# Kernel optimization log

Measured on AMD Instinct MI355X. Metric: run time of the kernel, lower is better.

Reference implementation:

```python
import jax, jax.numpy as jnp
import numpy as np

NPOS_MAX = 64
SCALE = 0.125  # head_dim ** -0.5


def setup_inputs() -> dict:
    key = jax.random.key(0)
    kq, kk, kv, kp, kw = jax.random.split(key, 5)
    B, S, D = 32, 1024, 64
    return {
        "q": jax.random.normal(kq, (B, S, D), dtype=jnp.float32),
        "k": jax.random.normal(kk, (B, S, D), dtype=jnp.float32),
        "v": jax.random.normal(kv, (B, S, D), dtype=jnp.float32),
        "pos_emb": jax.random.normal(kp, (1, D, NPOS_MAX), dtype=jnp.float32) * 0.02,
        "w_k": jax.random.normal(kw, (1, D, D), dtype=jnp.float32) * 0.02,
        "is_cope_k": 1,
    }


def reference(q, k, v, pos_emb, w_k, is_cope_k):
    # mode == 0: plain scaled QK^T
    attn_logits = jnp.einsum("bqd,bkd->bqk", q * SCALE, k)  # [B,S,S]
    gates = jax.nn.sigmoid(attn_logits)
    # reverse cumulative sum along the key axis (flip-cumsum-flip)
    pos = jnp.cumsum(gates[..., ::-1], axis=-1)[..., ::-1]
    pos = jnp.minimum(pos, NPOS_MAX - 1)
    pos_ceil = jnp.ceil(pos).astype(jnp.int32)
    pos_floor = jnp.floor(pos).astype(jnp.int32)
    base = q if is_cope_k else k
    logits_int = jnp.einsum("bsd,odn->bsn", base, pos_emb)  # [B,S,npos]
    logits_ceil = jnp.take_along_axis(logits_int, pos_ceil, axis=-1)
    logits_floor = jnp.take_along_axis(logits_int, pos_floor, axis=-1)
    w = pos - pos_floor.astype(pos.dtype)
    return logits_ceil * w + logits_floor * (1.0 - w)
```

## Files before the change

kernel.cpp:

```cpp
#include <hip/hip_runtime.h>

#define SLEN 1024
#define DDIM 64
#define NPOS 64
#define QROWS 16
#define QCOLS 256
#define COPE_SCALE 0.125f
#define GSTR 260
#define TSTR 66

typedef __bf16 bf16x8 __attribute__((ext_vector_type(8)));
typedef float f32x4 __attribute__((ext_vector_type(4)));

__device__ __forceinline__ unsigned short f2bf_hi(float x) {
    unsigned u = __builtin_bit_cast(unsigned, x);
    unsigned r = u + 0x7FFFu + ((u >> 16) & 1u);
    return (unsigned short)(r >> 16);
}
__device__ __forceinline__ float bf2f(unsigned short h) {
    unsigned u = ((unsigned)h) << 16;
    return __builtin_bit_cast(float, u);
}
struct U8 { ushort4 a, b; };
__device__ __forceinline__ bf16x8 pack8(const unsigned short* s) {
    U8 u = {{s[0], s[1], s[2], s[3]}, {s[4], s[5], s[6], s[7]}};
    return __builtin_bit_cast(bf16x8, u);
}

__global__ __launch_bounds__(256) void prep_kernel(
    const float* __restrict__ k,
    unsigned short* __restrict__ khi,
    unsigned short* __restrict__ klo,
    int n4)
{
    int i = blockIdx.x * 256 + threadIdx.x;
    if (i >= n4) return;
    float4 v = ((const float4*)k)[i];
    ushort4 h, l;
    h.x = f2bf_hi(v.x); l.x = f2bf_hi(v.x - bf2f(h.x));
    h.y = f2bf_hi(v.y); l.y = f2bf_hi(v.y - bf2f(h.y));
    h.z = f2bf_hi(v.z); l.z = f2bf_hi(v.z - bf2f(h.z));
    h.w = f2bf_hi(v.w); l.w = f2bf_hi(v.w - bf2f(h.w));
    ((ushort4*)khi)[i] = h;
    ((ushort4*)klo)[i] = l;
}

__global__ __launch_bounds__(256, 6) void cope_mfma_kernel(
    const float* __restrict__ q,
    const float* __restrict__ k,
    const float* __restrict__ pos_emb,
    const int*   __restrict__ is_cope_k,
    const unsigned short* __restrict__ khi,
    const unsigned short* __restrict__ klo,
    float*       __restrict__ out)
{
    __shared__ __align__(16) float G[QROWS * GSTR];
    __shared__ __align__(16) float tableL[QROWS * TSTR];
    __shared__ float Racc[QROWS];

    const int t = threadIdx.x;
    const int wave = t >> 6;
    const int lane = t & 63;
    const int quad = lane >> 4;
    const int nloc = lane & 15;
    const int blk = blockIdx.x;
    const int batch = blk >> 6;
    const int qbase = (blk & 63) * QROWS;

    if (t < QROWS) Racc[t] = 0.f;

    bf16x8 a_hi[2], a_lo[2];
    {
        const float* qrow = q + (size_t)(batch * SLEN + qbase + nloc) * DDIM + quad * 8;
        #pragma unroll
        for (int ks = 0; ks < 2; ++ks) {
            float4 v0 = *(const float4*)(qrow + ks * 32);
            float4 v1 = *(const float4*)(qrow + ks * 32 + 4);
            float xs[8] = {v0.x, v0.y, v0.z, v0.w, v1.x, v1.y, v1.z, v1.w};
            unsigned short hb[8], lb[8];
            #pragma unroll
            for (int j = 0; j < 8; ++j) {
                hb[j] = f2bf_hi(xs[j]);
                lb[j] = f2bf_hi(xs[j] - bf2f(hb[j]));
            }
            a_hi[ks] = pack8(hb);
            a_lo[ks] = pack8(lb);
        }
    }

    {
        const int icope = *is_cope_k;
        bf16x8 t_hi[2], t_lo[2];
        if (icope) {
            t_hi[0] = a_hi[0]; t_hi[1] = a_hi[1];
            t_lo[0] = a_lo[0]; t_lo[1] = a_lo[1];
        } else {
            size_t boff = (size_t)(batch * SLEN + qbase + nloc) * DDIM + quad * 8;
            t_hi[0] = __builtin_bit_cast(bf16x8, *(const uint4*)(khi + boff));
            t_hi[1] = __builtin_bit_cast(bf16x8, *(const uint4*)(khi + boff + 32));
            t_lo[0] = __builtin_bit_cast(bf16x8, *(const uint4*)(klo + boff));
            t_lo[1] = __builtin_bit_cast(bf16x8, *(const uint4*)(klo + boff + 32));
        }
        bf16x8 p_hi[2];
        #pragma unroll
        for (int ks = 0; ks < 2; ++ks) {
            unsigned short hb[8];
            #pragma unroll
            for (int j = 0; j < 8; ++j) {
                float pv = pos_emb[(quad * 8 + j + ks * 32) * NPOS + wave * 16 + nloc];
                hb[j] = f2bf_hi(pv);
            }
            p_hi[ks] = pack8(hb);
        }
        f32x4 tacc = {0.f, 0.f, 0.f, 0.f};
        tacc = __builtin_amdgcn_mfma_f32_16x16x32_bf16(t_hi[0], p_hi[0], tacc, 0, 0, 0);
        tacc = __builtin_amdgcn_mfma_f32_16x16x32_bf16(t_lo[0], p_hi[0], tacc, 0, 0, 0);
        tacc = __builtin_amdgcn_mfma_f32_16x16x32_bf16(t_hi[1], p_hi[1], tacc, 0, 0, 0);
        tacc = __builtin_amdgcn_mfma_f32_16x16x32_bf16(t_lo[1], p_hi[1], tacc, 0, 0, 0);
        #pragma unroll
        for (int reg = 0; reg < 4; ++reg)
            tableL[(quad * 4 + reg) * TSTR + wave * 16 + nloc] = tacc[reg];
    }

    int remaining = 0;
    for (int qi = 3; qi >= 0; --qi) {
        #pragma unroll
        for (int i = 0; i < 4; ++i) {
            const int tl = wave * 4 + i;
            size_t boff = (size_t)(batch * SLEN + qi * QCOLS + tl * 16 + nloc) * DDIM + quad * 8;
            uint4 bh0 = *(const uint4*)(khi + boff);
            uint4 bh1 = *(const uint4*)(khi + boff + 32);
            uint4 bl0 = *(const uint4*)(klo + boff);
            uint4 bl1 = *(const uint4*)(klo + boff + 32);
            f32x4 acc = {0.f, 0.f, 0.f, 0.f};
            acc = __builtin_amdgcn_mfma_f32_16x16x32_bf16(a_hi[0], __builtin_bit_cast(bf16x8, bh0), acc, 0, 0, 0);
            acc = __builtin_amdgcn_mfma_f32_16x16x32_bf16(a_lo[0], __builtin_bit_cast(bf16x8, bh0), acc, 0, 0, 0);
            acc = __builtin_amdgcn_mfma_f32_16x16x32_bf16(a_hi[0], __builtin_bit_cast(bf16x8, bl0), acc, 0, 0, 0);
            acc = __builtin_amdgcn_mfma_f32_16x16x32_bf16(a_hi[1], __builtin_bit_cast(bf16x8, bh1), acc, 0, 0, 0);
            acc = __builtin_amdgcn_mfma_f32_16x16x32_bf16(a_lo[1], __builtin_bit_cast(bf16x8, bh1), acc, 0, 0, 0);
            acc = __builtin_amdgcn_mfma_f32_16x16x32_bf16(a_hi[1], __builtin_bit_cast(bf16x8, bl1), acc, 0, 0, 0);
            #pragma unroll
            for (int reg = 0; reg < 4; ++reg) {
                float x = acc[reg] * COPE_SCALE;
                float g = __builtin_amdgcn_rcpf(1.0f + __expf(-x));
                G[(quad * 4 + reg) * GSTR + tl * 16 + nloc] = g;
            }
        }
        __syncthreads();

        #pragma unroll
        for (int rep = 0; rep < 4; ++rep) {
            const int row = wave * 4 + rep;
            const float roff = Racc[row];
            float4 gv = *(const float4*)&G[row * GSTR + lane * 4];
            float ls3 = gv.w;
            float ls2 = gv.z + ls3;
            float ls1 = gv.y + ls2;
            float ls0 = gv.x + ls1;
            const float T = ls0;
            float v = T;
            #pragma unroll
            for (int ofs = 1; ofs < 64; ofs <<= 1) {
                float u = __shfl_down(v, ofs);
                if (lane + ofs < 64) v += u;
            }
            if (lane == 0) Racc[row] = roff + v;
            const float E = (v - T) + roff;

            const float tabv = tableL[row * TSTR + lane];
            float dtabv = __shfl_down(tabv, 1) - tabv;
            if (lane == 63) dtabv = 0.f;
            float ls[4] = {ls0, ls1, ls2, ls3};
            float res[4];
            #pragma unroll
            for (int i = 0; i < 4; ++i) {
                float p = ls[i] + E;
                p = fminf(p, (float)(NPOS - 1));
                float pf = floorf(p);
                int fi = (int)pf;
                float w = p - pf;
                float tf = __shfl(tabv, fi);
                float td = __shfl(dtabv, fi);
                res[i] = tf + w * td;
            }
            float* orow = out + (size_t)(batch * SLEN + qbase + row) * SLEN + qi * QCOLS + lane * 4;
            f32x4 o = {res[0], res[1], res[2], res[3]};
            __builtin_nontemporal_store(o, (f32x4*)orow);
        }
        __syncthreads();

        float mn = Racc[0];
        #pragma unroll
        for (int r = 1; r < QROWS; ++r) mn = fminf(mn, Racc[r]);
        if (mn >= (float)(NPOS - 1)) { remaining = qi; break; }
    }

    if (remaining > 0) {
        const int ncols = remaining * QCOLS;
        #pragma unroll
        for (int rep = 0; rep < 4; ++rep) {
            const int row = wave * 4 + rep;
            const float v63 = tableL[row * TSTR + (NPOS - 1)];
            f32x4 bv = {v63, v63, v63, v63};
            float* orow = out + (size_t)(batch * SLEN + qbase + row) * SLEN;
            for (int c = lane * 4; c < ncols; c += 256)
                __builtin_nontemporal_store(bv, (f32x4*)(orow + c));
        }
    }
}

#define KTILE 128
#define KPAD 68
#define NTILES (SLEN / KTILE)
#define FQROWS 8

__global__ __launch_bounds__(256) void cope_fallback(
    const float* __restrict__ q,
    const float* __restrict__ k,
    const float* __restrict__ pos_emb,
    const int*   __restrict__ is_cope_k,
    float*       __restrict__ out)
{
    __shared__ __align__(16) float smem[KTILE * KPAD];
    __shared__ __align__(16) float qT[DDIM][FQROWS];
    __shared__ __align__(16) float baseT[DDIM][FQROWS];
    __shared__ __align__(16) float tableL2[FQROWS][NPOS];

    const int t = threadIdx.x;
    const int blk = blockIdx.x;
    const int batch = blk / (SLEN / FQROWS);
    const int qbase = (blk % (SLEN / FQROWS)) * FQROWS;
    const float* bsrc = (*is_cope_k) ? q : k;

    for (int i = t; i < FQROWS * DDIM; i += 256) {
        int r = i >> 6, d = i & 63;
        size_t gi = (size_t)(batch * SLEN + qbase + r) * DDIM + d;
        qT[d][r] = q[gi];
        baseT[d][r] = bsrc[gi];
    }
    __syncthreads();
    for (int i = t; i < FQROWS * NPOS; i += 256) {
        int r = i >> 6, n = i & 63;
        float a = 0.f;
        #pragma unroll
        for (int d = 0; d < DDIM; ++d) a += baseT[d][r] * pos_emb[d * NPOS + n];
        tableL2[r][n] = a;
    }
    const int jl = t & 127;
    const int qg = t >> 7;
    float acc[4][NTILES];
    #pragma unroll
    for (int r = 0; r < 4; ++r)
        #pragma unroll
        for (int tl = 0; tl < NTILES; ++tl) acc[r][tl] = 0.f;
    float (*kT)[KPAD] = (float (*)[KPAD])smem;
    const float* kbatch = k + (size_t)batch * SLEN * DDIM;
    #pragma unroll
    for (int tile = 0; tile < NTILES; ++tile) {
        __syncthreads();
        const float4* src = (const float4*)(kbatch + tile * KTILE * DDIM);
        #pragma unroll
        for (int i = 0; i < (KTILE * DDIM / 4) / 256; ++i) {
            int idx = i * 256 + t;
            int row = (idx * 4) >> 6;
            int col = (idx * 4) & 63;
            float4 vv = src[idx];
            *(float4*)&kT[row][col] = vv;
        }
        __syncthreads();
        #pragma unroll
        for (int d = 0; d < DDIM; d += 4) {
            float4 kv = *(const float4*)&kT[jl][d];
            float4 q0 = *(const float4*)&qT[d + 0][qg * 4];
            float4 q1 = *(const float4*)&qT[d + 1][qg * 4];
            float4 q2 = *(const float4*)&qT[d + 2][qg * 4];
            float4 q3 = *(const float4*)&qT[d + 3][qg * 4];
            acc[0][tile] += kv.x * q0.x + kv.y * q1.x + kv.z * q2.x + kv.w * q3.x;
            acc[1][tile] += kv.x * q0.y + kv.y * q1.y + kv.z * q2.y + kv.w * q3.y;
            acc[2][tile] += kv.x * q0.z + kv.y * q1.z + kv.z * q2.z + kv.w * q3.z;
            acc[3][tile] += kv.x * q0.w + kv.y * q1.w + kv.z * q2.w + kv.w * q3.w;
        }
    }
    __syncthreads();
    float (*G2)[SLEN] = (float (*)[SLEN])smem;
    #pragma unroll
    for (int r = 0; r < 4; ++r)
        #pragma unroll
        for (int tl = 0; tl < NTILES; ++tl) {
            float x = acc[r][tl] * COPE_SCALE;
            G2[qg * 4 + r][tl * KTILE + jl] = 1.0f / (1.0f + __expf(-x));
        }
    __syncthreads();
    const int wave = t >> 6;
    const int lane = t & 63;
    #pragma unroll
    for (int rep = 0; rep < 2; ++rep) {
        const int row = wave * 2 + rep;
        float g4[4][4];
        #pragma unroll
        for (int s = 0; s < 4; ++s) {
            float4 v = *(const float4*)&G2[row][s * 256 + lane * 4];
            g4[s][0] = v.x; g4[s][1] = v.y; g4[s][2] = v.z; g4[s][3] = v.w;
        }
        float ls[4][4], T[4];
        #pragma unroll
        for (int s = 0; s < 4; ++s) {
            float a = 0.f;
            #pragma unroll
            for (int i = 3; i >= 0; --i) { a += g4[s][i]; ls[s][i] = a; }
            T[s] = a;
        }
        float E[4], Stot[4];
        #pragma unroll
        for (int s = 0; s < 4; ++s) {
            float v = T[s];
            #pragma unroll
            for (int ofs = 1; ofs < 64; ofs <<= 1) {
                float u = __shfl_down(v, ofs);
                if (lane + ofs < 64) v += u;
            }
            E[s] = v - T[s];
            Stot[s] = __shfl(v, 0);
        }
        float segOff[4];
        segOff[3] = 0.f;
        segOff[2] = Stot[3];
        segOff[1] = Stot[3] + Stot[2];
        segOff[0] = Stot[3] + Stot[2] + Stot[1];
        const float* tab = tableL2[row];
        float* orow = out + (size_t)(batch * SLEN + qbase + row) * SLEN;
        #pragma unroll
        for (int s = 0; s < 4; ++s) {
            float res[4];
            #pragma unroll
            for (int i = 0; i < 4; ++i) {
                float p = ls[s][i] + E[s] + segOff[s];
                p = fminf(p, (float)(NPOS - 1));
                float pf = floorf(p);
                int fi = (int)pf;
                int ci = (int)ceilf(p);
                float w = p - pf;
                res[i] = tab[ci] * w + tab[fi] * (1.0f - w);
            }
            float4 o; o.x = res[0]; o.y = res[1]; o.z = res[2]; o.w = res[3];
            *(float4*)&orow[s * 256 + lane * 4] = o;
        }
    }
}

extern "C" void kernel_launch(void* const* d_in, const int* in_sizes, int n_in,
                              void* d_out, int out_size, void* d_ws, size_t ws_size,
                              hipStream_t stream) {
    const float* q        = (const float*)d_in[0];
    const float* k        = (const float*)d_in[1];
    const float* pos_emb  = (const float*)d_in[3];
    const int*   is_cope_k = (const int*)d_in[5];
    float* out = (float*)d_out;

    const int nk = in_sizes[1];
    const int B = in_sizes[0] / (SLEN * DDIM);
    const size_t ws_need = (size_t)nk * 2 * sizeof(unsigned short);

    if (ws_size >= ws_need) {
        unsigned short* khi = (unsigned short*)d_ws;
        unsigned short* klo = khi + nk;
        int n4 = nk / 4;
        prep_kernel<<<(n4 + 255) / 256, 256, 0, stream>>>(k, khi, klo, n4);
        cope_mfma_kernel<<<B * (SLEN / QROWS), 256, 0, stream>>>(
            q, k, pos_emb, is_cope_k, khi, klo, out);
    } else {
        cope_fallback<<<B * (SLEN / FQROWS), 256, 0, stream>>>(
            q, k, pos_emb, is_cope_k, out);
    }
}
```

Baseline: 173.8 us.

## Prep only last key quarter; split remaining keys to bf16 inline from fp32

The prep kernel now converts only the final 256-key chunk of each batch into hi/lo bf16 arrays instead of all keys. The main kernel splits the other chunks on the fly from fp32 k, and only when the early-exit check has not already fired. When is_cope_k is 0, the table base is also split inline from fp32. This cuts prep work and workspace traffic, since most chunks are usually skipped. The cost is extra VALU conversion work and twice-as-wide fp32 loads for any chunks that do get processed.

```diff
diff --git a/kernel.cpp b/kernel.cpp
--- a/kernel.cpp
+++ b/kernel.cpp
@@ -27,22 +27,58 @@
     return __builtin_bit_cast(bf16x8, u);
 }
 
-__global__ __launch_bounds__(256) void prep_kernel(
+__device__ __forceinline__ void load_split_f32(
+    const float* __restrict__ row, bf16x8 hi[2], bf16x8 lo[2])
+{
+    #pragma unroll
+    for (int ks = 0; ks < 2; ++ks) {
+        float4 v0 = *(const float4*)(row + ks * 32);
+        float4 v1 = *(const float4*)(row + ks * 32 + 4);
+        float xs[8] = {v0.x, v0.y, v0.z, v0.w, v1.x, v1.y, v1.z, v1.w};
+        unsigned short hb[8], lb[8];
+        #pragma unroll
+        for (int j = 0; j < 8; ++j) {
+            hb[j] = f2bf_hi(xs[j]);
+            lb[j] = f2bf_hi(xs[j] - bf2f(hb[j]));
+        }
+        hi[ks] = pack8(hb);
+        lo[ks] = pack8(lb);
+    }
+}
+
+__device__ __forceinline__ f32x4 qk6(const bf16x8 a_hi[2], const bf16x8 a_lo[2],
+                                     bf16x8 bh0, bf16x8 bh1, bf16x8 bl0, bf16x8 bl1)
+{
+    f32x4 acc = {0.f, 0.f, 0.f, 0.f};
+    acc = __builtin_amdgcn_mfma_f32_16x16x32_bf16(a_hi[0], bh0, acc, 0, 0, 0);
+    acc = __builtin_amdgcn_mfma_f32_16x16x32_bf16(a_lo[0], bh0, acc, 0, 0, 0);
+    acc = __builtin_amdgcn_mfma_f32_16x16x32_bf16(a_hi[0], bl0, acc, 0, 0, 0);
+    acc = __builtin_amdgcn_mfma_f32_16x16x32_bf16(a_hi[1], bh1, acc, 0, 0, 0);
+    acc = __builtin_amdgcn_mfma_f32_16x16x32_bf16(a_lo[1], bh1, acc, 0, 0, 0);
+    acc = __builtin_amdgcn_mfma_f32_16x16x32_bf16(a_hi[1], bl1, acc, 0, 0, 0);
+    return acc;
+}
+
+__global__ __launch_bounds__(256) void prep_kernel_q3(
     const float* __restrict__ k,
     unsigned short* __restrict__ khi,
     unsigned short* __restrict__ klo,
-    int n4)
+    int B)
 {
+    const int per_batch = QCOLS * DDIM / 4;
     int i = blockIdx.x * 256 + threadIdx.x;
-    if (i >= n4) return;
-    float4 v = ((const float4*)k)[i];
+    if (i >= B * per_batch) return;
+    int b = i / per_batch;
+    int off = i - b * per_batch;
+    size_t idx4 = ((size_t)b * SLEN + 3 * QCOLS) * (DDIM / 4) + off;
+    float4 v = ((const float4*)k)[idx4];
     ushort4 h, l;
     h.x = f2bf_hi(v.x); l.x = f2bf_hi(v.x - bf2f(h.x));
     h.y = f2bf_hi(v.y); l.y = f2bf_hi(v.y - bf2f(h.y));
     h.z = f2bf_hi(v.z); l.z = f2bf_hi(v.z - bf2f(h.z));
     h.w = f2bf_hi(v.w); l.w = f2bf_hi(v.w - bf2f(h.w));
-    ((ushort4*)khi)[i] = h;
-    ((ushort4*)klo)[i] = l;
+    ((ushort4*)khi)[idx4] = h;
+    ((ushort4*)klo)[idx4] = l;
 }
 
 __global__ __launch_bounds__(256, 6) void cope_mfma_kernel(
@@ -70,23 +106,8 @@
     if (t < QROWS) Racc[t] = 0.f;
 
     bf16x8 a_hi[2], a_lo[2];
-    {
-        const float* qrow = q + (size_t)(batch * SLEN + qbase + nloc) * DDIM + quad * 8;
-        #pragma unroll
-        for (int ks = 0; ks < 2; ++ks) {
-            float4 v0 = *(const float4*)(qrow + ks * 32);
-            float4 v1 = *(const float4*)(qrow + ks * 32 + 4);
-            float xs[8] = {v0.x, v0.y, v0.z, v0.w, v1.x, v1.y, v1.z, v1.w};
-            unsigned short hb[8], lb[8];
-            #pragma unroll
-            for (int j = 0; j < 8; ++j) {
-                hb[j] = f2bf_hi(xs[j]);
-                lb[j] = f2bf_hi(xs[j] - bf2f(hb[j]));
-            }
-            a_hi[ks] = pack8(hb);
-            a_lo[ks] = pack8(lb);
-        }
-    }
+    load_split_f32(q + (size_t)(batch * SLEN + qbase + nloc) * DDIM + quad * 8,
+                   a_hi, a_lo);
 
     {
         const int icope = *is_cope_k;
@@ -95,11 +116,8 @@
             t_hi[0] = a_hi[0]; t_hi[1] = a_hi[1];
             t_lo[0] = a_lo[0]; t_lo[1] = a_lo[1];
         } else {
-            size_t boff = (size_t)(batch * SLEN + qbase + nloc) * DDIM + quad * 8;
-            t_hi[0] = __builtin_bit_cast(bf16x8, *(const uint4*)(khi + boff));
-            t_hi[1] = __builtin_bit_cast(bf16x8, *(const uint4*)(khi + boff + 32));
-            t_lo[0] = __builtin_bit_cast(bf16x8, *(const uint4*)(klo + boff));
-            t_lo[1] = __builtin_bit_cast(bf16x8, *(const uint4*)(klo + boff + 32));
+            load_split_f32(k + (size_t)(batch * SLEN + qbase + nloc) * DDIM + quad * 8,
+                           t_hi, t_lo);
         }
         bf16x8 p_hi[2];
         #pragma unroll
@@ -122,23 +140,16 @@
             tableL[(quad * 4 + reg) * TSTR + wave * 16 + nloc] = tacc[reg];
     }
 
-    int remaining = 0;
-    for (int qi = 3; qi >= 0; --qi) {
-        #pragma unroll
+    {
+        #pragma unroll 2
         for (int i = 0; i < 4; ++i) {
             const int tl = wave * 4 + i;
-            size_t boff = (size_t)(batch * SLEN + qi * QCOLS + tl * 16 + nloc) * DDIM + quad * 8;
-            uint4 bh0 = *(const uint4*)(khi + boff);
-            uint4 bh1 = *(const uint4*)(khi + boff + 32);
-            uint4 bl0 = *(const uint4*)(klo + boff);
-            uint4 bl1 = *(const uint4*)(klo + boff + 32);
-            f32x4 acc = {0.f, 0.f, 0.f, 0.f};
-            acc = __builtin_amdgcn_mfma_f32_16x16x32_bf16(a_hi[0], __builtin_bit_cast(bf16x8, bh0), acc, 0, 0, 0);
-            acc = __builtin_amdgcn_mfma_f32_16x16x32_bf16(a_lo[0], __builtin_bit_cast(bf16x8, bh0), acc, 0, 0, 0);
-            acc = __builtin_amdgcn_mfma_f32_16x16x32_bf16(a_hi[0], __builtin_bit_cast(bf16x8, bl0), acc, 0, 0, 0);
-            acc = __builtin_amdgcn_mfma_f32_16x16x32_bf16(a_hi[1], __builtin_bit_cast(bf16x8, bh1), acc, 0, 0, 0);
-            acc = __builtin_amdgcn_mfma_f32_16x16x32_bf16(a_lo[1], __builtin_bit_cast(bf16x8, bh1), acc, 0, 0, 0);
-            acc = __builtin_amdgcn_mfma_f32_16x16x32_bf16(a_hi[1], __builtin_bit_cast(bf16x8, bl1), acc, 0, 0, 0);
+            size_t boff = (size_t)(batch * SLEN + 3 * QCOLS + tl * 16 + nloc) * DDIM + quad * 8;
+            bf16x8 bh0 = __builtin_bit_cast(bf16x8, *(const uint4*)(khi + boff));
+            bf16x8 bh1 = __builtin_bit_cast(bf16x8, *(const uint4*)(khi + boff + 32));
+            bf16x8 bl0 = __builtin_bit_cast(bf16x8, *(const uint4*)(klo + boff));
+            bf16x8 bl1 = __builtin_bit_cast(bf16x8, *(const uint4*)(klo + boff + 32));
+            f32x4 acc = qk6(a_hi, a_lo, bh0, bh1, bl0, bl1);
             #pragma unroll
             for (int reg = 0; reg < 4; ++reg) {
                 float x = acc[reg] * COPE_SCALE;
@@ -147,7 +158,10 @@
             }
         }
         __syncthreads();
-
+    }
+
+    int remaining = 3;
+    for (int qi = 3; ; --qi) {
         #pragma unroll
         for (int rep = 0; rep < 4; ++rep) {
             const int row = wave * 4 + rep;
@@ -193,6 +207,24 @@
         #pragma unroll
         for (int r = 1; r < QROWS; ++r) mn = fminf(mn, Racc[r]);
         if (mn >= (float)(NPOS - 1)) { remaining = qi; break; }
+        if (qi == 0) { remaining = 0; break; }
+
+        #pragma unroll 2
+        for (int i = 0; i < 4; ++i) {
+            const int tl = wave * 4 + i;
+            bf16x8 b_hi[2], b_lo[2];
+            load_split_f32(
+                k + (size_t)(batch * SLEN + (qi - 1) * QCOLS + tl * 16 + nloc) * DDIM + quad * 8,
+                b_hi, b_lo);
+            f32x4 acc = qk6(a_hi, a_lo, b_hi[0], b_hi[1], b_lo[0], b_lo[1]);
+            #pragma unroll
+            for (int reg = 0; reg < 4; ++reg) {
+                float x = acc[reg] * COPE_SCALE;
+                float g = __builtin_amdgcn_rcpf(1.0f + __expf(-x));
+                G[(quad * 4 + reg) * GSTR + tl * 16 + nloc] = g;
+            }
+        }
+        __syncthreads();
     }
 
     if (remaining > 0) {
@@ -364,8 +396,8 @@
     if (ws_size >= ws_need) {
         unsigned short* khi = (unsigned short*)d_ws;
         unsigned short* klo = khi + nk;
-        int n4 = nk / 4;
-        prep_kernel<<<(n4 + 255) / 256, 256, 0, stream>>>(k, khi, klo, n4);
+        const int n_q3 = B * (QCOLS * DDIM / 4);
+        prep_kernel_q3<<<(n_q3 + 255) / 256, 256, 0, stream>>>(k, khi, klo, B);
         cope_mfma_kernel<<<B * (SLEN / QROWS), 256, 0, stream>>>(
             q, k, pos_emb, is_cope_k, khi, klo, out);
     } else {
```

Measured after the change: 176.9 us. About the same (+1.8%).
